# Kernel optimization log

Hardware: AMD Instinct MI355X
Metric: run time of the kernel (lower is better)

## Reference

```python
import jax, jax.numpy as jnp
import numpy as np

B, S, D = 1, 2048, 1024
H, KVH, HD = 16, 4, 64   # D == H * HD; GQA repeat = H // KVH = 4
E, A, I = 8, 2, 3584
EPS = 1e-05
ROPE_BASE = 10000.0


def setup_inputs() -> dict:
    key = jax.random.key(0)
    ks = jax.random.split(key, 8)
    s = 0.02  # weight init scale
    x = jax.random.normal(ks[0], (B, S, D), jnp.float32)
    wqkv = jax.random.normal(ks[1], ((H + 2 * KVH) * HD, D), jnp.float32) * s
    wo = jax.random.normal(ks[2], (D, D), jnp.float32) * s
    gate_w = jax.random.normal(ks[3], (E, D), jnp.float32) * s
    w1 = jax.random.normal(ks[4], (E, I, D), jnp.float32) * s
    w2 = jax.random.normal(ks[5], (E, D, I), jnp.float32) * s
    w3 = jax.random.normal(ks[6], (E, I, D), jnp.float32) * s
    attn_norm_w = jnp.ones((D,), jnp.float32)
    ffn_norm_w = jnp.ones((D,), jnp.float32)
    # rotary table: [S, HD//2, 2] = (cos, sin)
    half = HD // 2
    inv_freq = 1.0 / (ROPE_BASE ** (np.arange(half, dtype=np.float32) / half))
    ang = np.outer(np.arange(S, dtype=np.float32), inv_freq)
    freqs_cis = jnp.asarray(np.stack([np.cos(ang), np.sin(ang)], -1), jnp.float32)
    mask = jnp.tril(jnp.ones((S, S), bool))  # causal, True = attend
    return dict(x=x, wqkv=wqkv, wo=wo, gate_w=gate_w, w1=w1, w2=w2, w3=w3,
                attn_norm_w=attn_norm_w, ffn_norm_w=ffn_norm_w,
                freqs_cis=freqs_cis, mask=mask)


def rmsnorm(x, w, eps=EPS):
    xf = x.astype(jnp.float32)
    n = xf * jax.lax.rsqrt(jnp.mean(xf * xf, axis=-1, keepdims=True) + eps)
    return n.astype(x.dtype) * w


def rope(x, freqs_cis):
    # x: [B, S, h, HD]; freqs_cis: [S, HD//2, 2]
    xs = x.reshape(*x.shape[:-1], -1, 2)
    f = freqs_cis.reshape(1, xs.shape[1], 1, xs.shape[3], 2)
    out = jnp.stack([xs[..., 0] * f[..., 0] - xs[..., 1] * f[..., 1],
                     xs[..., 1] * f[..., 0] + xs[..., 0] * f[..., 1]], axis=-1)
    return out.reshape(x.shape).astype(x.dtype)


def reference(x, wqkv, wo, gate_w, w1, w2, w3, attn_norm_w, ffn_norm_w, freqs_cis, mask):
    # ---- attention ----
    hn = rmsnorm(x, attn_norm_w)
    qkv = hn @ wqkv.T
    kv_size = KVH * HD
    q, k, v = jnp.split(qkv, [D, D + kv_size], axis=-1)
    q = rope(q.reshape(B, S, H, HD), freqs_cis).transpose(0, 2, 1, 3)    # [B,H,S,HD]
    k = rope(k.reshape(B, S, KVH, HD), freqs_cis).transpose(0, 2, 1, 3)  # [B,KVH,S,HD]
    v = v.reshape(B, S, KVH, HD).transpose(0, 2, 1, 3)
    rep = H // KVH
    k = jnp.repeat(k, rep, axis=1)
    v = jnp.repeat(v, rep, axis=1)
    scores = jnp.einsum('bhqd,bhkd->bhqk', q, k) / np.float32(np.sqrt(HD))
    scores = jnp.where(mask, scores, jnp.float32(-1e30))
    probs = jax.nn.softmax(scores, axis=-1)
    y = jnp.einsum('bhqk,bhkd->bhqd', probs, v)
    y = y.transpose(0, 2, 1, 3).reshape(B, S, D)
    h = x + y @ wo.T
    # ---- MoE FFN ----
    hf = rmsnorm(h, ffn_norm_w).reshape(-1, D)            # [T, D]
    gates = jax.nn.softmax(hf @ gate_w.T, axis=-1)        # [T, E]
    ew, ei = jax.lax.top_k(gates, A)                      # [T, A]
    ew = ew / jnp.sum(ew, axis=-1, keepdims=True)
    # math identical to gathering w1/w3/w2 per token, but computed as
    # dense all-expert GEMMs followed by an output gather (no weight replication)
    x1 = jax.nn.silu(jnp.einsum('td,eod->teo', hf, w1))   # [T, E, I]
    x3 = jnp.einsum('td,eod->teo', hf, w3)
    out_all = jnp.einsum('teo,edo->ted', x1 * x3, w2)     # [T, E, D]
    eo = jnp.take_along_axis(out_all, ei[:, :, None], axis=1)  # [T, A, D]
    ffn = jnp.einsum('tad,ta->td', eo, ew).reshape(B, S, D)
    return h + ffn
```

## Files before the change

kernel.cpp:

```cpp
#include <hip/hip_runtime.h>
#include <hip/hip_bf16.h>
#include <math.h>

#define SS 2048
#define DD 1024
#define NH 16
#define NKVH 4
#define HDIM 64
#define NE 8
#define NI 3584
#define QKVN 1536
#define PCAP 5120
#define NTILEMAX 40

typedef unsigned short u16;
typedef short short8 __attribute__((ext_vector_type(8)));
typedef float floatx4 __attribute__((ext_vector_type(4)));

__device__ inline u16 f2bf(float f) {
  unsigned u = __float_as_uint(f);
  unsigned r = u + 0x7fffu + ((u >> 16) & 1u);
  return (u16)(r >> 16);
}
__device__ inline float bf2f(u16 h) { return __uint_as_float((unsigned)h << 16); }

__global__ void f32_to_bf16_kernel(const float* __restrict__ in, u16* __restrict__ out, int n4) {
  int i = blockIdx.x * 256 + threadIdx.x;
  if (i >= n4) return;
  float4 v = ((const float4*)in)[i];
  ((ushort4*)out)[i] = make_ushort4(f2bf(v.x), f2bf(v.y), f2bf(v.z), f2bf(v.w));
}

__global__ void rmsnorm_kernel(const float* __restrict__ x, const float* __restrict__ w,
                               float* __restrict__ o32, u16* __restrict__ o16) {
  int row = blockIdx.x;
  int t = threadIdx.x;
  float4 v = ((const float4*)(x + (size_t)row * DD))[t];
  float ss = v.x * v.x + v.y * v.y + v.z * v.z + v.w * v.w;
  for (int o = 32; o > 0; o >>= 1) ss += __shfl_xor(ss, o);
  __shared__ float red[4];
  if ((t & 63) == 0) red[t >> 6] = ss;
  __syncthreads();
  float tot = red[0] + red[1] + red[2] + red[3];
  float r = rsqrtf(tot * (1.f / DD) + 1e-5f);
  float4 wv = ((const float4*)w)[t];
  float4 o;
  o.x = v.x * r * wv.x; o.y = v.y * r * wv.y; o.z = v.z * r * wv.z; o.w = v.w * r * wv.w;
  if (o32) ((float4*)(o32 + (size_t)row * DD))[t] = o;
  if (o16) ((ushort4*)(o16 + (size_t)row * DD))[t] =
      make_ushort4(f2bf(o.x), f2bf(o.y), f2bf(o.z), f2bf(o.w));
}

__global__ __launch_bounds__(256) void gemm128(
    const u16* __restrict__ A, const u16* __restrict__ B,
    float* __restrict__ C, const float* __restrict__ addend, int N, int K) {
  __shared__ u16 As[128 * 32];
  __shared__ u16 Bs[128 * 32];
  int tid = threadIdx.x;
  int bm = blockIdx.x * 128;
  int bn = blockIdx.y * 128;
  const u16* Ag = A + (size_t)bm * K;
  const u16* Bg = B + (size_t)bn * K;
  int wave = tid >> 6, lane = tid & 63;
  int wm = wave >> 1, wn = wave & 1;
  int ml = lane & 15, quad = lane >> 4;

  floatx4 acc[4][4];
#pragma unroll
  for (int i = 0; i < 4; i++)
#pragma unroll
    for (int j = 0; j < 4; j++) acc[i][j] = (floatx4){0.f, 0.f, 0.f, 0.f};

  for (int k0 = 0; k0 < K; k0 += 32) {
#pragma unroll
    for (int r = 0; r < 2; r++) {
      int s = tid + r * 256;
      int row = s >> 2, kc = (s & 3) * 8;
      __builtin_amdgcn_global_load_lds(
          (const __attribute__((address_space(1))) unsigned*)(Ag + (size_t)row * K + k0 + kc),
          (__attribute__((address_space(3))) unsigned*)(As + s * 8), 16, 0, 0);
      __builtin_amdgcn_global_load_lds(
          (const __attribute__((address_space(1))) unsigned*)(Bg + (size_t)row * K + k0 + kc),
          (__attribute__((address_space(3))) unsigned*)(Bs + s * 8), 16, 0, 0);
    }
    __syncthreads();
    short8 a[4], b[4];
#pragma unroll
    for (int i = 0; i < 4; i++)
      a[i] = *(const short8*)(As + ((wm * 64 + i * 16 + ml) * 32 + quad * 8));
#pragma unroll
    for (int j = 0; j < 4; j++)
      b[j] = *(const short8*)(Bs + ((wn * 64 + j * 16 + ml) * 32 + quad * 8));
#pragma unroll
    for (int i = 0; i < 4; i++)
#pragma unroll
      for (int j = 0; j < 4; j++)
        acc[i][j] = __builtin_amdgcn_mfma_f32_16x16x32_bf16(a[i], b[j], acc[i][j], 0, 0, 0);
    __syncthreads();
  }
#pragma unroll
  for (int i = 0; i < 4; i++) {
#pragma unroll
    for (int j = 0; j < 4; j++) {
#pragma unroll
      for (int r = 0; r < 4; r++) {
        int row = bm + wm * 64 + i * 16 + quad * 4 + r;
        int col = bn + wn * 64 + j * 16 + ml;
        size_t idx = (size_t)row * N + col;
        float v = acc[i][j][r];
        if (addend) v += addend[idx];
        C[idx] = v;
      }
    }
  }
}

__global__ __launch_bounds__(256, 3) void moe_stage1(
    const u16* __restrict__ xslot, const u16* __restrict__ w1b, const u16* __restrict__ w3b,
    const int* __restrict__ tmap, u16* __restrict__ x13) {
  __shared__ u16 As[128 * 32];
  __shared__ u16 B1s[64 * 32];
  __shared__ u16 B3s[64 * 32];
  int tI = blockIdx.y % NTILEMAX;
  int cI = blockIdx.x + 8 * (blockIdx.y / NTILEMAX);
  if (tI >= tmap[0]) return;
  int entry = tmap[1 + tI];
  int e = entry & 7;
  int row0 = (entry >> 3) * 128;
  int bn = cI * 64;
  const u16* Ag = xslot + (size_t)row0 * DD;
  const u16* B1g = w1b + (size_t)e * NI * DD + (size_t)bn * DD;
  const u16* B3g = w3b + (size_t)e * NI * DD + (size_t)bn * DD;
  int tid = threadIdx.x, wave = tid >> 6, lane = tid & 63;
  int wm = wave >> 1, wn = wave & 1;
  int ml = lane & 15, quad = lane >> 4;

  floatx4 acc1[4][2], acc3[4][2];
#pragma unroll
  for (int i = 0; i < 4; i++)
#pragma unroll
    for (int j = 0; j < 2; j++) {
      acc1[i][j] = (floatx4){0.f, 0.f, 0.f, 0.f};
      acc3[i][j] = (floatx4){0.f, 0.f, 0.f, 0.f};
    }

  for (int k0 = 0; k0 < DD; k0 += 32) {
#pragma unroll
    for (int r = 0; r < 2; r++) {
      int s = tid + r * 256;
      int row = s >> 2, kc = (s & 3) * 8;
      __builtin_amdgcn_global_load_lds(
          (const __attribute__((address_space(1))) unsigned*)(Ag + (size_t)row * DD + k0 + kc),
          (__attribute__((address_space(3))) unsigned*)(As + s * 8), 16, 0, 0);
    }
    {
      int row = tid >> 2, kc = (tid & 3) * 8;
      __builtin_amdgcn_global_load_lds(
          (const __attribute__((address_space(1))) unsigned*)(B1g + (size_t)row * DD + k0 + kc),
          (__attribute__((address_space(3))) unsigned*)(B1s + tid * 8), 16, 0, 0);
      __builtin_amdgcn_global_load_lds(
          (const __attribute__((address_space(1))) unsigned*)(B3g + (size_t)row * DD + k0 + kc),
          (__attribute__((address_space(3))) unsigned*)(B3s + tid * 8), 16, 0, 0);
    }
    __syncthreads();
    short8 a[4], b1[2], b3[2];
#pragma unroll
    for (int i = 0; i < 4; i++)
      a[i] = *(const short8*)(As + ((wm * 64 + i * 16 + ml) * 32 + quad * 8));
#pragma unroll
    for (int j = 0; j < 2; j++) {
      b1[j] = *(const short8*)(B1s + ((wn * 32 + j * 16 + ml) * 32 + quad * 8));
      b3[j] = *(const short8*)(B3s + ((wn * 32 + j * 16 + ml) * 32 + quad * 8));
    }
#pragma unroll
    for (int i = 0; i < 4; i++)
#pragma unroll
      for (int j = 0; j < 2; j++) {
        acc1[i][j] = __builtin_amdgcn_mfma_f32_16x16x32_bf16(a[i], b1[j], acc1[i][j], 0, 0, 0);
        acc3[i][j] = __builtin_amdgcn_mfma_f32_16x16x32_bf16(a[i], b3[j], acc3[i][j], 0, 0, 0);
      }
    __syncthreads();
  }
#pragma unroll
  for (int i = 0; i < 4; i++) {
#pragma unroll
    for (int j = 0; j < 2; j++) {
#pragma unroll
      for (int r = 0; r < 4; r++) {
        int row = row0 + wm * 64 + i * 16 + quad * 4 + r;
        int col = bn + wn * 32 + j * 16 + ml;
        float v1 = acc1[i][j][r], v3 = acc3[i][j][r];
        float sil = v1 / (1.f + __expf(-v1));
        x13[(size_t)row * NI + col] = f2bf(sil * v3);
      }
    }
  }
}

__global__ __launch_bounds__(256) void moe_stage2(
    const u16* __restrict__ x13, const u16* __restrict__ w2b,
    const int* __restrict__ tmap, float* __restrict__ pbuf) {
  __shared__ u16 As[128 * 32];
  __shared__ u16 Bs[128 * 32];
  int tI = blockIdx.y % NTILEMAX;
  int kh = blockIdx.y / NTILEMAX;
  int nt = blockIdx.x;
  if (tI >= tmap[0]) return;
  int entry = tmap[1 + tI];
  int e = entry & 7;
  int row0 = (entry >> 3) * 128;
  int bn = nt * 128;
  int kbeg = kh * (NI / 2), kend = kbeg + NI / 2;
  const u16* Ag = x13 + (size_t)row0 * NI;
  const u16* Bg = w2b + (size_t)e * DD * NI + (size_t)bn * NI;
  float* Cp = pbuf + (size_t)kh * PCAP * DD;
  int tid = threadIdx.x, wave = tid >> 6, lane = tid & 63;
  int wm = wave >> 1, wn = wave & 1;
  int ml = lane & 15, quad = lane >> 4;

  floatx4 acc[4][4];
#pragma unroll
  for (int i = 0; i < 4; i++)
#pragma unroll
    for (int j = 0; j < 4; j++) acc[i][j] = (floatx4){0.f, 0.f, 0.f, 0.f};

  for (int k0 = kbeg; k0 < kend; k0 += 32) {
#pragma unroll
    for (int r = 0; r < 2; r++) {
      int s = tid + r * 256;
      int row = s >> 2, kc = (s & 3) * 8;
      __builtin_amdgcn_global_load_lds(
          (const __attribute__((address_space(1))) unsigned*)(Ag + (size_t)row * NI + k0 + kc),
          (__attribute__((address_space(3))) unsigned*)(As + s * 8), 16, 0, 0);
      __builtin_amdgcn_global_load_lds(
          (const __attribute__((address_space(1))) unsigned*)(Bg + (size_t)row * NI + k0 + kc),
          (__attribute__((address_space(3))) unsigned*)(Bs + s * 8), 16, 0, 0);
    }
    __syncthreads();
    short8 a[4], b[4];
#pragma unroll
    for (int i = 0; i < 4; i++)
      a[i] = *(const short8*)(As + ((wm * 64 + i * 16 + ml) * 32 + quad * 8));
#pragma unroll
    for (int j = 0; j < 4; j++)
      b[j] = *(const short8*)(Bs + ((wn * 64 + j * 16 + ml) * 32 + quad * 8));
#pragma unroll
    for (int i = 0; i < 4; i++)
#pragma unroll
      for (int j = 0; j < 4; j++)
        acc[i][j] = __builtin_amdgcn_mfma_f32_16x16x32_bf16(a[i], b[j], acc[i][j], 0, 0, 0);
    __syncthreads();
  }
#pragma unroll
  for (int i = 0; i < 4; i++) {
#pragma unroll
    for (int j = 0; j < 4; j++) {
#pragma unroll
      for (int r = 0; r < 4; r++) {
        int row = row0 + wm * 64 + i * 16 + quad * 4 + r;
        int col = bn + wn * 64 + j * 16 + ml;
        Cp[(size_t)row * DD + col] = acc[i][j][r];
      }
    }
  }
}

__global__ void rope_kernel(const float* __restrict__ qkv, const float* __restrict__ freqs,
                            u16* __restrict__ qT, u16* __restrict__ kT) {
  int s = blockIdx.x;
  int tid = threadIdx.x;
#pragma unroll
  for (int r = 0; r < 2; r++) {
    int tt = r * 256 + tid;
    int hh = tt >> 5, i = tt & 31;
    const float* p = qkv + (size_t)s * QKVN + hh * 64 + 2 * i;
    float c = freqs[(s * 32 + i) * 2], sn = freqs[(s * 32 + i) * 2 + 1];
    float x0 = p[0], x1 = p[1];
    float r0 = (x0 * c - x1 * sn) * 0.125f;
    float r1 = (x1 * c + x0 * sn) * 0.125f;
    unsigned pk = (unsigned)f2bf(r0) | ((unsigned)f2bf(r1) << 16);
    *(unsigned*)(qT + ((size_t)hh * SS + s) * 64 + 2 * i) = pk;
  }
  if (tid < 128) {
    int hh = tid >> 5, i = tid & 31;
    const float* p = qkv + (size_t)s * QKVN + DD + hh * 64 + 2 * i;
    float c = freqs[(s * 32 + i) * 2], sn = freqs[(s * 32 + i) * 2 + 1];
    float x0 = p[0], x1 = p[1];
    float r0 = x0 * c - x1 * sn;
    float r1 = x1 * c + x0 * sn;
    unsigned pk = (unsigned)f2bf(r0) | ((unsigned)f2bf(r1) << 16);
    *(unsigned*)(kT + ((size_t)hh * SS + s) * 64 + 2 * i) = pk;
  }
}

__global__ void vtrans_kernel(const float* __restrict__ qkv, u16* __restrict__ vT2) {
  __shared__ u16 tile[64][65];
  int bs = blockIdx.x * 64;
  int bc = blockIdx.y * 64;
  int tid = threadIdx.x;
#pragma unroll
  for (int it = 0; it < 4; it++) {
    int idx = it * 256 + tid;
    int r = idx >> 4, c4 = idx & 15;
    float4 v = *(const float4*)(qkv + (size_t)(bs + r) * QKVN + DD + 256 + bc + c4 * 4);
    tile[r][c4 * 4 + 0] = f2bf(v.x);
    tile[r][c4 * 4 + 1] = f2bf(v.y);
    tile[r][c4 * 4 + 2] = f2bf(v.z);
    tile[r][c4 * 4 + 3] = f2bf(v.w);
  }
  __syncthreads();
#pragma unroll
  for (int it = 0; it < 4; it++) {
    int idx = it * 256 + tid;
    int cc = idx >> 4, s4 = idx & 15;
    ushort4 o = make_ushort4(tile[s4 * 4 + 0][cc], tile[s4 * 4 + 1][cc],
                             tile[s4 * 4 + 2][cc], tile[s4 * 4 + 3][cc]);
    *(ushort4*)(vT2 + (size_t)(bc + cc) * SS + bs + s4 * 4) = o;
  }
}

#define BQ 128
#define BKV 64
__global__ __launch_bounds__(256) void attn_flash(const u16* __restrict__ qT,
                                                  const u16* __restrict__ kT,
                                                  const u16* __restrict__ vT2,
                                                  u16* __restrict__ y) {
  __shared__ u16 Ks[2 * 64 * 32];
  __shared__ u16 Vs[2 * 64 * 32];
  __shared__ u16 Ps[2 * 128 * 36];
  int t = blockIdx.x;
  int h = blockIdx.y;
  int kvh = h >> 2;
  int bq = t * BQ;
  int tid = threadIdx.x, wave = tid >> 6, lane = tid & 63;
  int ml = lane & 15, quad = lane >> 4;

  short8 qf[2][2];
#pragma unroll
  for (int i = 0; i < 2; i++)
#pragma unroll
    for (int c = 0; c < 2; c++)
      qf[i][c] = *(const short8*)(qT + ((size_t)h * SS + bq + wave * 32 + i * 16 + ml) * 64 +
                                  c * 32 + quad * 8);

  float m_i[2][4], l_i[2][4];
  floatx4 o_acc[2][4];
#pragma unroll
  for (int i = 0; i < 2; i++)
#pragma unroll
    for (int r = 0; r < 4; r++) {
      m_i[i][r] = -1e30f;
      l_i[i][r] = 0.f;
      o_acc[i][r] = (floatx4){0.f, 0.f, 0.f, 0.f};
    }

  int nkv = 2 * t + 2;
  for (int kt = 0; kt < nkv; kt++) {
    int bk = kt * BKV;
    __syncthreads();
#pragma unroll
    for (int r = 0; r < 2; r++) {
      int ch = r * 256 + tid;
      int c = ch >> 8, srow = (ch >> 2) & 63, o8 = ch & 3;
      __builtin_amdgcn_global_load_lds(
          (const __attribute__((address_space(1))) unsigned*)(
              kT + ((size_t)kvh * SS + bk + srow) * 64 + c * 32 + o8 * 8),
          (__attribute__((address_space(3))) unsigned*)(Ks + ch * 8), 16, 0, 0);
      __builtin_amdgcn_global_load_lds(
          (const __attribute__((address_space(1))) unsigned*)(
              vT2 + ((size_t)kvh * 64 + srow) * SS + bk + c * 32 + o8 * 8),
          (__attribute__((address_space(3))) unsigned*)(Vs + ch * 8), 16, 0, 0);
    }
    __syncthreads();

    floatx4 s_acc[2][4];
#pragma unroll
    for (int i = 0; i < 2; i++)
#pragma unroll
      for (int j = 0; j < 4; j++) s_acc[i][j] = (floatx4){0.f, 0.f, 0.f, 0.f};
#pragma unroll
    for (int c = 0; c < 2; c++) {
#pragma unroll
      for (int jk = 0; jk < 4; jk++) {
        short8 kf = *(const short8*)(Ks + c * 2048 + (jk * 16 + ml) * 32 + quad * 8);
#pragma unroll
        for (int i = 0; i < 2; i++)
          s_acc[i][jk] = __builtin_amdgcn_mfma_f32_16x16x32_bf16(qf[i][c], kf, s_acc[i][jk], 0, 0, 0);
      }
    }
    if (bk + BKV - 1 > bq) {
#pragma unroll
      for (int i = 0; i < 2; i++)
#pragma unroll
        for (int jk = 0; jk < 4; jk++)
#pragma unroll
          for (int r = 0; r < 4; r++) {
            int row = bq + wave * 32 + i * 16 + quad * 4 + r;
            int col = bk + jk * 16 + ml;
            if (col > row) s_acc[i][jk][r] = -1e30f;
          }
    }
#pragma unroll
    for (int i = 0; i < 2; i++) {
#pragma unroll
      for (int r = 0; r < 4; r++) {
        float mx = -1e30f;
#pragma unroll
        for (int jk = 0; jk < 4; jk++) mx = fmaxf(mx, s_acc[i][jk][r]);
        for (int o = 1; o < 16; o <<= 1) mx = fmaxf(mx, __shfl_xor(mx, o));
        float mnew = fmaxf(m_i[i][r], mx);
        float alpha = __expf(m_i[i][r] - mnew);
        m_i[i][r] = mnew;
        float rs = 0.f;
#pragma unroll
        for (int jk = 0; jk < 4; jk++) {
          float p = __expf(s_acc[i][jk][r] - mnew);
          s_acc[i][jk][r] = p;
          rs += p;
        }
        for (int o = 1; o < 16; o <<= 1) rs += __shfl_xor(rs, o);
        l_i[i][r] = l_i[i][r] * alpha + rs;
#pragma unroll
        for (int jd = 0; jd < 4; jd++) o_acc[i][jd][r] *= alpha;
      }
    }
#pragma unroll
    for (int i = 0; i < 2; i++)
#pragma unroll
      for (int jk = 0; jk < 4; jk++)
#pragma unroll
        for (int r = 0; r < 4; r++) {
          int row = wave * 32 + i * 16 + quad * 4 + r;
          int col = jk * 16 + ml;
          Ps[(col >> 5) * (128 * 36) + row * 36 + (col & 31)] = f2bf(s_acc[i][jk][r]);
        }
#pragma unroll
    for (int kc = 0; kc < 2; kc++) {
      short8 pf[2];
#pragma unroll
      for (int i = 0; i < 2; i++)
        pf[i] = *(const short8*)(Ps + kc * (128 * 36) + (wave * 32 + i * 16 + ml) * 36 + quad * 8);
#pragma unroll
      for (int jd = 0; jd < 4; jd++) {
        short8 vf = *(const short8*)(Vs + kc * 2048 + (jd * 16 + ml) * 32 + quad * 8);
#pragma unroll
        for (int i = 0; i < 2; i++)
          o_acc[i][jd] = __builtin_amdgcn_mfma_f32_16x16x32_bf16(pf[i], vf, o_acc[i][jd], 0, 0, 0);
      }
    }
  }
#pragma unroll
  for (int i = 0; i < 2; i++) {
    float inv[4];
#pragma unroll
    for (int r = 0; r < 4; r++) inv[r] = 1.f / l_i[i][r];
#pragma unroll
    for (int jd = 0; jd < 4; jd++)
#pragma unroll
      for (int r = 0; r < 4; r++) {
        int row = bq + wave * 32 + i * 16 + quad * 4 + r;
        int col = h * 64 + jd * 16 + ml;
        y[(size_t)row * DD + col] = f2bf(o_acc[i][jd][r] * inv[r]);
      }
  }
}

__global__ __launch_bounds__(64) void gate_kernel(const float* __restrict__ hf,
                                                  const float* __restrict__ gw,
                                                  int* __restrict__ ei, float* __restrict__ ew,
                                                  int* __restrict__ cnt) {
  int t = blockIdx.x;
  int lane = threadIdx.x;
  const float* xr = hf + (size_t)t * DD;
  float acc[NE] = {};
  for (int c = 0; c < DD / 64; c++) {
    float xv = xr[lane + 64 * c];
#pragma unroll
    for (int e = 0; e < NE; e++) acc[e] += xv * gw[e * DD + lane + 64 * c];
  }
#pragma unroll
  for (int e = 0; e < NE; e++)
    for (int o = 32; o > 0; o >>= 1) acc[e] += __shfl_xor(acc[e], o);
  if (lane == 0) {
    float mx = acc[0];
    for (int e = 1; e < NE; e++) mx = fmaxf(mx, acc[e]);
    float p[NE], sum = 0.f;
    for (int e = 0; e < NE; e++) { p[e] = __expf(acc[e] - mx); sum += p[e]; }
    for (int e = 0; e < NE; e++) p[e] /= sum;
    int i0 = 0;
    for (int e = 1; e < NE; e++) if (p[e] > p[i0]) i0 = e;
    int i1 = (i0 == 0) ? 1 : 0;
    for (int e = 0; e < NE; e++) if (e != i0 && p[e] > p[i1]) i1 = e;
    float w0 = p[i0], w1 = p[i1], s = w0 + w1;
    ei[t * 2] = i0; ei[t * 2 + 1] = i1;
    ew[t * 2] = w0 / s; ew[t * 2 + 1] = w1 / s;
    atomicAdd(&cnt[i0], 1);
    atomicAdd(&cnt[i1], 1);
  }
}

__global__ void zero_cnt_kernel(int* cnt) {
  if (threadIdx.x < NE) cnt[threadIdx.x] = 0;
}

__global__ void prefix_kernel(const int* __restrict__ cnt, int* __restrict__ poff,
                              int* __restrict__ fill) {
  if (threadIdx.x == 0) {
    int pacc = 0;
    for (int e = 0; e < NE; e++) {
      poff[e] = pacc;
      pacc += (cnt[e] + 127) & ~127;
    }
    poff[NE] = pacc;
  }
  if (threadIdx.x < NE) fill[threadIdx.x] = 0;
}

__global__ void tilemap_kernel(const int* __restrict__ poff, int* __restrict__ tmap) {
  if (threadIdx.x == 0) {
    int n = 0;
    for (int e = 0; e < NE; e++) {
      int r0 = poff[e] >> 7, r1 = poff[e + 1] >> 7;
      for (int r = r0; r < r1; r++) tmap[1 + n++] = (r << 3) | e;
    }
    tmap[0] = n;
  }
}

__global__ void fill_kernel(const int* __restrict__ ei, const int* __restrict__ poff,
                            int* __restrict__ fill, int* __restrict__ slot_of) {
  int t = blockIdx.x * blockDim.x + threadIdx.x;
  if (t >= SS) return;
  for (int a = 0; a < 2; a++) {
    int e = ei[t * 2 + a];
    int pos = atomicAdd(&fill[e], 1);
    slot_of[t * 2 + a] = poff[e] + pos;
  }
}

__global__ void gather_kernel(const u16* __restrict__ hf16, const int* __restrict__ slot_of,
                              u16* __restrict__ xslot) {
  int t = blockIdx.x;
  uint2 v = ((const uint2*)(hf16 + (size_t)t * DD))[threadIdx.x];
  for (int a = 0; a < 2; a++) {
    int slot = slot_of[t * 2 + a];
    ((uint2*)(xslot + (size_t)slot * DD))[threadIdx.x] = v;
  }
}

__global__ void final_kernel(const float* __restrict__ h, const float* __restrict__ p0,
                             const float* __restrict__ p1, const int* __restrict__ slot_of,
                             const float* __restrict__ ew, float* __restrict__ out) {
  int t = blockIdx.x;
  int s0 = slot_of[t * 2], s1 = slot_of[t * 2 + 1];
  float w0 = ew[t * 2], w1 = ew[t * 2 + 1];
  float4 hv = ((const float4*)(h + (size_t)t * DD))[threadIdx.x];
  float4 a0 = ((const float4*)(p0 + (size_t)s0 * DD))[threadIdx.x];
  float4 a1 = ((const float4*)(p1 + (size_t)s0 * DD))[threadIdx.x];
  float4 b0 = ((const float4*)(p0 + (size_t)s1 * DD))[threadIdx.x];
  float4 b1 = ((const float4*)(p1 + (size_t)s1 * DD))[threadIdx.x];
  float4 o;
  o.x = hv.x + w0 * (a0.x + a1.x) + w1 * (b0.x + b1.x);
  o.y = hv.y + w0 * (a0.y + a1.y) + w1 * (b0.y + b1.y);
  o.z = hv.z + w0 * (a0.z + a1.z) + w1 * (b0.z + b1.z);
  o.w = hv.w + w0 * (a0.w + a1.w) + w1 * (b0.w + b1.w);
  ((float4*)(out + (size_t)t * DD))[threadIdx.x] = o;
}

extern "C" void kernel_launch(void* const* d_in, const int* in_sizes, int n_in,
                              void* d_out, int out_size, void* d_ws, size_t ws_size,
                              hipStream_t stream) {
  const float* x = (const float*)d_in[0];
  const float* wqkv = (const float*)d_in[1];
  const float* wo = (const float*)d_in[2];
  const float* gate_w = (const float*)d_in[3];
  const float* w1 = (const float*)d_in[4];
  const float* w2 = (const float*)d_in[5];
  const float* w3 = (const float*)d_in[6];
  const float* attn_norm_w = (const float*)d_in[7];
  const float* ffn_norm_w = (const float*)d_in[8];
  const float* freqs = (const float*)d_in[9];
  float* out = (float*)d_out;

  char* ws = (char*)d_ws;
  size_t off = 0;
  auto alloc = [&](size_t bytes) -> char* {
    char* p = ws + off;
    off = (off + bytes + 255) & ~(size_t)255;
    return p;
  };
  u16* hn16    = (u16*)alloc((size_t)SS * DD * 2);
  float* qkv   = (float*)alloc((size_t)SS * QKVN * 4);
  u16* y16     = (u16*)alloc((size_t)SS * DD * 2);
  float* hbuf  = (float*)alloc((size_t)SS * DD * 4);
  float* hf    = (float*)alloc((size_t)SS * DD * 4);
  u16* hf16    = (u16*)alloc((size_t)SS * DD * 2);
  u16* kT      = (u16*)alloc((size_t)NKVH * SS * HDIM * 2);
  u16* vT2     = (u16*)alloc((size_t)NKVH * HDIM * SS * 2);
  u16* wqkv16  = (u16*)alloc((size_t)QKVN * DD * 2);
  u16* wo16    = (u16*)alloc((size_t)DD * DD * 2);
  u16* w1_16   = (u16*)alloc((size_t)NE * NI * DD * 2);
  u16* w3_16   = (u16*)alloc((size_t)NE * NI * DD * 2);
  u16* w2_16   = (u16*)alloc((size_t)NE * DD * NI * 2);
  u16* xslot   = (u16*)alloc((size_t)PCAP * DD * 2);
  u16* x13     = (u16*)alloc((size_t)PCAP * NI * 2);
  float* pbuf  = (float*)alloc((size_t)2 * PCAP * DD * 4);
  int* ei      = (int*)alloc((size_t)SS * 2 * 4);
  float* ew    = (float*)alloc((size_t)SS * 2 * 4);
  int* slot_of = (int*)alloc((size_t)SS * 2 * 4);
  int* cnt     = (int*)alloc(NE * 4);
  int* poff    = (int*)alloc((NE + 1) * 4);
  int* fill    = (int*)alloc(NE * 4);
  int* tmap    = (int*)alloc((NTILEMAX + 1) * 4);
  u16* qT      = hn16;

  auto conv = [&](const float* src, u16* dst, size_t n) {
    int n4 = (int)(n / 4);
    f32_to_bf16_kernel<<<(n4 + 255) / 256, 256, 0, stream>>>(src, dst, n4);
  };

  zero_cnt_kernel<<<1, 64, 0, stream>>>(cnt);
  conv(wqkv, wqkv16, (size_t)QKVN * DD);
  conv(wo, wo16, (size_t)DD * DD);
  conv(w1, w1_16, (size_t)NE * NI * DD);
  conv(w3, w3_16, (size_t)NE * NI * DD);
  conv(w2, w2_16, (size_t)NE * DD * NI);

  rmsnorm_kernel<<<SS, 256, 0, stream>>>(x, attn_norm_w, nullptr, hn16);
  gemm128<<<dim3(SS / 128, QKVN / 128), 256, 0, stream>>>(hn16, wqkv16, qkv, nullptr, QKVN, DD);
  rope_kernel<<<SS, 256, 0, stream>>>(qkv, freqs, qT, kT);
  vtrans_kernel<<<dim3(SS / 64, 4), 256, 0, stream>>>(qkv, vT2);
  attn_flash<<<dim3(SS / BQ, NH), 256, 0, stream>>>(qT, kT, vT2, y16);
  gemm128<<<dim3(SS / 128, DD / 128), 256, 0, stream>>>(y16, wo16, hbuf, x, DD, DD);

  rmsnorm_kernel<<<SS, 256, 0, stream>>>(hbuf, ffn_norm_w, hf, hf16);
  gate_kernel<<<SS, 64, 0, stream>>>(hf, gate_w, ei, ew, cnt);
  prefix_kernel<<<1, 64, 0, stream>>>(cnt, poff, fill);
  tilemap_kernel<<<1, 64, 0, stream>>>(poff, tmap);
  fill_kernel<<<(SS + 255) / 256, 256, 0, stream>>>(ei, poff, fill, slot_of);
  gather_kernel<<<SS, 256, 0, stream>>>(hf16, slot_of, xslot);
  moe_stage1<<<dim3(8, (NI / 64 / 8) * NTILEMAX), 256, 0, stream>>>(xslot, w1_16, w3_16, tmap, x13);
  moe_stage2<<<dim3(8, 2 * NTILEMAX), 256, 0, stream>>>(x13, w2_16, tmap, pbuf);
  final_kernel<<<SS, 256, 0, stream>>>(hbuf, pbuf, pbuf + (size_t)PCAP * DD, slot_of, ew, out);
}
```

Baseline: 797.6 us.

## Fuse fp32-to-bf16 expert weight conversion into MoE GEMM loads with swizzled LDS

```diff
diff --git a/kernel.cpp b/kernel.cpp
--- a/kernel.cpp
+++ b/kernel.cpp
@@ -116,7 +116,7 @@
 }
 
 __global__ __launch_bounds__(256, 3) void moe_stage1(
-    const u16* __restrict__ xslot, const u16* __restrict__ w1b, const u16* __restrict__ w3b,
+    const u16* __restrict__ xslot, const float* __restrict__ w1f, const float* __restrict__ w3f,
     const int* __restrict__ tmap, u16* __restrict__ x13) {
   __shared__ u16 As[128 * 32];
   __shared__ u16 B1s[64 * 32];
@@ -129,12 +129,17 @@
   int row0 = (entry >> 3) * 128;
   int bn = cI * 64;
   const u16* Ag = xslot + (size_t)row0 * DD;
-  const u16* B1g = w1b + (size_t)e * NI * DD + (size_t)bn * DD;
-  const u16* B3g = w3b + (size_t)e * NI * DD + (size_t)bn * DD;
+  const float* B1g = w1f + (size_t)e * NI * DD + (size_t)bn * DD;
+  const float* B3g = w3f + (size_t)e * NI * DD + (size_t)bn * DD;
   int tid = threadIdx.x, wave = tid >> 6, lane = tid & 63;
   int wm = wave >> 1, wn = wave & 1;
   int ml = lane & 15, quad = lane >> 4;
 
+  int brow = tid >> 2, bc8 = tid & 3;
+  int wbyte = (brow * 64 + bc8 * 16) ^ ((brow & 6) << 3);
+  const float* b1p = B1g + (size_t)brow * DD + bc8 * 8;
+  const float* b3p = B3g + (size_t)brow * DD + bc8 * 8;
+
   floatx4 acc1[4][2], acc3[4][2];
 #pragma unroll
   for (int i = 0; i < 4; i++)
@@ -148,29 +153,41 @@
 #pragma unroll
     for (int r = 0; r < 2; r++) {
       int s = tid + r * 256;
-      int row = s >> 2, kc = (s & 3) * 8;
+      int row = s >> 2;
+      int sc = (s & 3) ^ ((row >> 1) & 3);
       __builtin_amdgcn_global_load_lds(
-          (const __attribute__((address_space(1))) unsigned*)(Ag + (size_t)row * DD + k0 + kc),
+          (const __attribute__((address_space(1))) unsigned*)(Ag + (size_t)row * DD + k0 + sc * 8),
           (__attribute__((address_space(3))) unsigned*)(As + s * 8), 16, 0, 0);
     }
-    {
-      int row = tid >> 2, kc = (tid & 3) * 8;
-      __builtin_amdgcn_global_load_lds(
-          (const __attribute__((address_space(1))) unsigned*)(B1g + (size_t)row * DD + k0 + kc),
-          (__attribute__((address_space(3))) unsigned*)(B1s + tid * 8), 16, 0, 0);
-      __builtin_amdgcn_global_load_lds(
-          (const __attribute__((address_space(1))) unsigned*)(B3g + (size_t)row * DD + k0 + kc),
-          (__attribute__((address_space(3))) unsigned*)(B3s + tid * 8), 16, 0, 0);
-    }
+    float4 u0 = *(const float4*)(b1p + k0);
+    float4 u1 = *(const float4*)(b1p + k0 + 4);
+    float4 v0 = *(const float4*)(b3p + k0);
+    float4 v1 = *(const float4*)(b3p + k0 + 4);
+    short8 pb1, pb3;
+    pb1[0] = (short)f2bf(u0.x); pb1[1] = (short)f2bf(u0.y);
+    pb1[2] = (short)f2bf(u0.z); pb1[3] = (short)f2bf(u0.w);
+    pb1[4] = (short)f2bf(u1.x); pb1[5] = (short)f2bf(u1.y);
+    pb1[6] = (short)f2bf(u1.z); pb1[7] = (short)f2bf(u1.w);
+    pb3[0] = (short)f2bf(v0.x); pb3[1] = (short)f2bf(v0.y);
+    pb3[2] = (short)f2bf(v0.z); pb3[3] = (short)f2bf(v0.w);
+    pb3[4] = (short)f2bf(v1.x); pb3[5] = (short)f2bf(v1.y);
+    pb3[6] = (short)f2bf(v1.z); pb3[7] = (short)f2bf(v1.w);
+    *(short8*)((char*)B1s + wbyte) = pb1;
+    *(short8*)((char*)B3s + wbyte) = pb3;
     __syncthreads();
     short8 a[4], b1[2], b3[2];
 #pragma unroll
-    for (int i = 0; i < 4; i++)
-      a[i] = *(const short8*)(As + ((wm * 64 + i * 16 + ml) * 32 + quad * 8));
+    for (int i = 0; i < 4; i++) {
+      int row = wm * 64 + i * 16 + ml;
+      int rb = (row * 64 + quad * 16) ^ ((row & 6) << 3);
+      a[i] = *(const short8*)((const char*)As + rb);
+    }
 #pragma unroll
     for (int j = 0; j < 2; j++) {
-      b1[j] = *(const short8*)(B1s + ((wn * 32 + j * 16 + ml) * 32 + quad * 8));
-      b3[j] = *(const short8*)(B3s + ((wn * 32 + j * 16 + ml) * 32 + quad * 8));
+      int rr = wn * 32 + j * 16 + ml;
+      int rb = (rr * 64 + quad * 16) ^ ((rr & 6) << 3);
+      b1[j] = *(const short8*)((const char*)B1s + rb);
+      b3[j] = *(const short8*)((const char*)B3s + rb);
     }
 #pragma unroll
     for (int i = 0; i < 4; i++)
@@ -197,68 +214,84 @@
   }
 }
 
-__global__ __launch_bounds__(256) void moe_stage2(
-    const u16* __restrict__ x13, const u16* __restrict__ w2b,
+__global__ __launch_bounds__(256, 3) void moe_stage2(
+    const u16* __restrict__ x13, const float* __restrict__ w2f,
     const int* __restrict__ tmap, float* __restrict__ pbuf) {
   __shared__ u16 As[128 * 32];
-  __shared__ u16 Bs[128 * 32];
+  __shared__ u16 Bs[64 * 32];
   int tI = blockIdx.y % NTILEMAX;
-  int kh = blockIdx.y / NTILEMAX;
-  int nt = blockIdx.x;
+  int g = blockIdx.x + 8 * (blockIdx.y / NTILEMAX);
+  int nt = g & 15, kh = g >> 4;
   if (tI >= tmap[0]) return;
   int entry = tmap[1 + tI];
   int e = entry & 7;
   int row0 = (entry >> 3) * 128;
-  int bn = nt * 128;
+  int bn = nt * 64;
   int kbeg = kh * (NI / 2), kend = kbeg + NI / 2;
   const u16* Ag = x13 + (size_t)row0 * NI;
-  const u16* Bg = w2b + (size_t)e * DD * NI + (size_t)bn * NI;
+  const float* Bg = w2f + (size_t)e * DD * NI + (size_t)bn * NI;
   float* Cp = pbuf + (size_t)kh * PCAP * DD;
   int tid = threadIdx.x, wave = tid >> 6, lane = tid & 63;
   int wm = wave >> 1, wn = wave & 1;
   int ml = lane & 15, quad = lane >> 4;
 
-  floatx4 acc[4][4];
+  int brow = tid >> 2, bc8 = tid & 3;
+  int wbyte = (brow * 64 + bc8 * 16) ^ ((brow & 6) << 3);
+  const float* bp = Bg + (size_t)brow * NI + bc8 * 8;
+
+  floatx4 acc[4][2];
 #pragma unroll
   for (int i = 0; i < 4; i++)
 #pragma unroll
-    for (int j = 0; j < 4; j++) acc[i][j] = (floatx4){0.f, 0.f, 0.f, 0.f};
+    for (int j = 0; j < 2; j++) acc[i][j] = (floatx4){0.f, 0.f, 0.f, 0.f};
 
   for (int k0 = kbeg; k0 < kend; k0 += 32) {
 #pragma unroll
     for (int r = 0; r < 2; r++) {
       int s = tid + r * 256;
-      int row = s >> 2, kc = (s & 3) * 8;
+      int row = s >> 2;
+      int sc = (s & 3) ^ ((row >> 1) & 3);
       __builtin_amdgcn_global_load_lds(
-          (const __attribute__((address_space(1))) unsigned*)(Ag + (size_t)row * NI + k0 + kc),
+          (const __attribute__((address_space(1))) unsigned*)(Ag + (size_t)row * NI + k0 + sc * 8),
           (__attribute__((address_space(3))) unsigned*)(As + s * 8), 16, 0, 0);
-      __builtin_amdgcn_global_load_lds(
-          (const __attribute__((address_space(1))) unsigned*)(Bg + (size_t)row * NI + k0 + kc),
-          (__attribute__((address_space(3))) unsigned*)(Bs + s * 8), 16, 0, 0);
-    }
-    __syncthreads();
-    short8 a[4], b[4];
+    }
+    float4 u0 = *(const float4*)(bp + k0);
+    float4 u1 = *(const float4*)(bp + k0 + 4);
+    short8 pb;
+    pb[0] = (short)f2bf(u0.x); pb[1] = (short)f2bf(u0.y);
+    pb[2] = (short)f2bf(u0.z); pb[3] = (short)f2bf(u0.w);
+    pb[4] = (short)f2bf(u1.x); pb[5] = (short)f2bf(u1.y);
+    pb[6] = (short)f2bf(u1.z); pb[7] = (short)f2bf(u1.w);
+    *(short8*)((char*)Bs + wbyte) = pb;
+    __syncthreads();
+    short8 a[4], b[2];
+#pragma unroll
+    for (int i = 0; i < 4; i++) {
+      int row = wm * 64 + i * 16 + ml;
+      int rb = (row * 64 + quad * 16) ^ ((row & 6) << 3);
+      a[i] = *(const short8*)((const char*)As + rb);
+    }
+#pragma unroll
+    for (int j = 0; j < 2; j++) {
+      int rr = wn * 32 + j * 16 + ml;
+      int rb = (rr * 64 + quad * 16) ^ ((rr & 6) << 3);
+      b[j] = *(const short8*)((const char*)Bs + rb);
+    }
 #pragma unroll
     for (int i = 0; i < 4; i++)
-      a[i] = *(const short8*)(As + ((wm * 64 + i * 16 + ml) * 32 + quad * 8));
-#pragma unroll
-    for (int j = 0; j < 4; j++)
-      b[j] = *(const short8*)(Bs + ((wn * 64 + j * 16 + ml) * 32 + quad * 8));
-#pragma unroll
-    for (int i = 0; i < 4; i++)
-#pragma unroll
-      for (int j = 0; j < 4; j++)
+#pragma unroll
+      for (int j = 0; j < 2; j++)
         acc[i][j] = __builtin_amdgcn_mfma_f32_16x16x32_bf16(a[i], b[j], acc[i][j], 0, 0, 0);
     __syncthreads();
   }
 #pragma unroll
   for (int i = 0; i < 4; i++) {
 #pragma unroll
-    for (int j = 0; j < 4; j++) {
+    for (int j = 0; j < 2; j++) {
 #pragma unroll
       for (int r = 0; r < 4; r++) {
         int row = row0 + wm * 64 + i * 16 + quad * 4 + r;
-        int col = bn + wn * 64 + j * 16 + ml;
+        int col = bn + wn * 32 + j * 16 + ml;
         Cp[(size_t)row * DD + col] = acc[i][j][r];
       }
     }
@@ -599,9 +632,6 @@
   u16* vT2     = (u16*)alloc((size_t)NKVH * HDIM * SS * 2);
   u16* wqkv16  = (u16*)alloc((size_t)QKVN * DD * 2);
   u16* wo16    = (u16*)alloc((size_t)DD * DD * 2);
-  u16* w1_16   = (u16*)alloc((size_t)NE * NI * DD * 2);
-  u16* w3_16   = (u16*)alloc((size_t)NE * NI * DD * 2);
-  u16* w2_16   = (u16*)alloc((size_t)NE * DD * NI * 2);
   u16* xslot   = (u16*)alloc((size_t)PCAP * DD * 2);
   u16* x13     = (u16*)alloc((size_t)PCAP * NI * 2);
   float* pbuf  = (float*)alloc((size_t)2 * PCAP * DD * 4);
@@ -622,9 +652,6 @@
   zero_cnt_kernel<<<1, 64, 0, stream>>>(cnt);
   conv(wqkv, wqkv16, (size_t)QKVN * DD);
   conv(wo, wo16, (size_t)DD * DD);
-  conv(w1, w1_16, (size_t)NE * NI * DD);
-  conv(w3, w3_16, (size_t)NE * NI * DD);
-  conv(w2, w2_16, (size_t)NE * DD * NI);
 
   rmsnorm_kernel<<<SS, 256, 0, stream>>>(x, attn_norm_w, nullptr, hn16);
   gemm128<<<dim3(SS / 128, QKVN / 128), 256, 0, stream>>>(hn16, wqkv16, qkv, nullptr, QKVN, DD);
@@ -639,7 +666,7 @@
   tilemap_kernel<<<1, 64, 0, stream>>>(poff, tmap);
   fill_kernel<<<(SS + 255) / 256, 256, 0, stream>>>(ei, poff, fill, slot_of);
   gather_kernel<<<SS, 256, 0, stream>>>(hf16, slot_of, xslot);
-  moe_stage1<<<dim3(8, (NI / 64 / 8) * NTILEMAX), 256, 0, stream>>>(xslot, w1_16, w3_16, tmap, x13);
-  moe_stage2<<<dim3(8, 2 * NTILEMAX), 256, 0, stream>>>(x13, w2_16, tmap, pbuf);
+  moe_stage1<<<dim3(8, (NI / 64 / 8) * NTILEMAX), 256, 0, stream>>>(xslot, w1, w3, tmap, x13);
+  moe_stage2<<<dim3(8, 4 * NTILEMAX), 256, 0, stream>>>(x13, w2, tmap, pbuf);
   final_kernel<<<SS, 256, 0, stream>>>(hbuf, pbuf, pbuf + (size_t)PCAP * DD, slot_of, ew, out);
 }
```

New measurement: 762.2 us. 1.05x faster.
